# Kernel optimization log

Measured on AMD Instinct MI355X. Metric: run time of the kernel, lower is better.

## Reference

```python
import jax, jax.numpy as jnp
import numpy as np

H = 64   # hidden_size
I = 4    # input_size
O = 1    # output_size

def setup_inputs() -> dict:
    key = jax.random.key(0)
    ks = jax.random.split(key, 7)
    B, T = 1024, 1024
    s = 1.0 / np.sqrt(H)
    x = jax.random.normal(ks[0], (B, T, I), dtype=jnp.float32)
    # PyTorch nn.LSTM params, gate order (i, f, g, o)
    W_ih = jax.random.uniform(ks[1], (4 * H, I), minval=-s, maxval=s, dtype=jnp.float32)
    W_hh = jax.random.uniform(ks[2], (4 * H, H), minval=-s, maxval=s, dtype=jnp.float32)
    b_ih = jax.random.uniform(ks[3], (4 * H,), minval=-s, maxval=s, dtype=jnp.float32)
    b_hh = jax.random.uniform(ks[4], (4 * H,), minval=-s, maxval=s, dtype=jnp.float32)
    W_fc = jax.random.uniform(ks[5], (O, H), minval=-s, maxval=s, dtype=jnp.float32)
    b_fc = jax.random.uniform(ks[6], (O,), minval=-s, maxval=s, dtype=jnp.float32)
    return {"x": x, "W_ih": W_ih, "W_hh": W_hh, "b_ih": b_ih, "b_hh": b_hh,
            "W_fc": W_fc, "b_fc": b_fc}

def _lstm(x, W_ih, W_hh, b_ih, b_hh):
    B, T, _ = x.shape
    # precompute input contribution for all timesteps: [T, B, 4H]
    xg = (jnp.einsum('bti,gi->btg', x, W_ih) + b_ih + b_hh).transpose(1, 0, 2)

    def step(carry, xt):
        h, c = carry
        g = xt + h @ W_hh.T                     # [B, 4H]
        i, f, gg, o = jnp.split(g, 4, axis=-1)  # torch gate order i,f,g,o
        i = jax.nn.sigmoid(i)
        f = jax.nn.sigmoid(f)
        gg = jnp.tanh(gg)
        o = jax.nn.sigmoid(o)
        c = f * c + i * gg
        h = o * jnp.tanh(c)
        return (h, c), h

    h0 = jnp.zeros((B, H), dtype=x.dtype)
    c0 = jnp.zeros((B, H), dtype=x.dtype)
    _, hs = jax.lax.scan(step, (h0, c0), xg)    # hs: [T, B, H]
    return hs.transpose(1, 0, 2)                # [B, T, H]

def reference(x, W_ih, W_hh, b_ih, b_hh, W_fc, b_fc):
    out = _lstm(x, W_ih, W_hh, b_ih, b_hh)      # [B, T, H]
    # dropout in eval mode == identity (deterministic reference)
    return out @ W_fc.T + b_fc                  # [B, T, 1]
```

## Files before the change

### kernel.cpp

```cpp
#include <hip/hip_runtime.h>

#define TLEN  1024
#define HN    64
#define LOG2E 1.4426950408889634f

typedef __fp16 half2v __attribute__((ext_vector_type(2)));


#define FOR16A(X) \
    X(0) X(1) X(2) X(3) X(4) X(5) X(6) X(7) \
    X(8) X(9) X(10) X(11) X(12) X(13) X(14) X(15)
#define FOR16B(X) \
    X(16) X(17) X(18) X(19) X(20) X(21) X(22) X(23) \
    X(24) X(25) X(26) X(27) X(28) X(29) X(30) X(31)
#define FOR32(X) FOR16A(X) FOR16B(X)

__global__ __launch_bounds__(64, 1)
void lstm_dot2(const float* __restrict__ x,
               const float* __restrict__ W_ih,
               const float* __restrict__ W_hh,
               const float* __restrict__ b_ih,
               const float* __restrict__ b_hh,
               const float* __restrict__ W_fc,
               const float* __restrict__ b_fc,
               float* __restrict__ out)
{
    const int b = blockIdx.x;
    const int g = threadIdx.x;

    __shared__ float ring[64][65];

    const float* wr_i = W_hh + (0 * HN + g) * HN;
    const float* wr_f = W_hh + (1 * HN + g) * HN;
    const float* wr_g = W_hh + (2 * HN + g) * HN;
    const float* wr_o = W_hh + (3 * HN + g) * HN;

#define DECL(j) half2v pi##j, pf##j, pg##j, po##j;
    FOR32(DECL)
#undef DECL

#define LOADW(j) \
    pi##j = __builtin_amdgcn_cvt_pkrtz(wr_i[j] * LOG2E, wr_i[(j) + 32] * LOG2E); \
    pf##j = __builtin_amdgcn_cvt_pkrtz(wr_f[j] * LOG2E, wr_f[(j) + 32] * LOG2E); \
    pg##j = __builtin_amdgcn_cvt_pkrtz(wr_g[j] * (2.0f * LOG2E), \
                                       wr_g[(j) + 32] * (2.0f * LOG2E)); \
    po##j = __builtin_amdgcn_cvt_pkrtz(wr_o[j] * LOG2E, wr_o[(j) + 32] * LOG2E); \
    asm volatile("" : "+v"(pi##j), "+v"(pf##j), "+v"(pg##j), "+v"(po##j));
    FOR32(LOADW)
#undef LOADW

    half2v wip0 = __builtin_amdgcn_cvt_pkrtz(W_ih[(0 * HN + g) * 4 + 0] * LOG2E,
                                             W_ih[(0 * HN + g) * 4 + 1] * LOG2E);
    half2v wip1 = __builtin_amdgcn_cvt_pkrtz(W_ih[(0 * HN + g) * 4 + 2] * LOG2E,
                                             W_ih[(0 * HN + g) * 4 + 3] * LOG2E);
    half2v wfp0 = __builtin_amdgcn_cvt_pkrtz(W_ih[(1 * HN + g) * 4 + 0] * LOG2E,
                                             W_ih[(1 * HN + g) * 4 + 1] * LOG2E);
    half2v wfp1 = __builtin_amdgcn_cvt_pkrtz(W_ih[(1 * HN + g) * 4 + 2] * LOG2E,
                                             W_ih[(1 * HN + g) * 4 + 3] * LOG2E);
    half2v wgp0 = __builtin_amdgcn_cvt_pkrtz(W_ih[(2 * HN + g) * 4 + 0] * 2.0f * LOG2E,
                                             W_ih[(2 * HN + g) * 4 + 1] * 2.0f * LOG2E);
    half2v wgp1 = __builtin_amdgcn_cvt_pkrtz(W_ih[(2 * HN + g) * 4 + 2] * 2.0f * LOG2E,
                                             W_ih[(2 * HN + g) * 4 + 3] * 2.0f * LOG2E);
    half2v wop0 = __builtin_amdgcn_cvt_pkrtz(W_ih[(3 * HN + g) * 4 + 0] * LOG2E,
                                             W_ih[(3 * HN + g) * 4 + 1] * LOG2E);
    half2v wop1 = __builtin_amdgcn_cvt_pkrtz(W_ih[(3 * HN + g) * 4 + 2] * LOG2E,
                                             W_ih[(3 * HN + g) * 4 + 3] * LOG2E);

    const float bias_i = (b_ih[0 * HN + g] + b_hh[0 * HN + g]) * LOG2E;
    const float bias_f = (b_ih[1 * HN + g] + b_hh[1 * HN + g]) * LOG2E;
    const float bias_g = (b_ih[2 * HN + g] + b_hh[2 * HN + g]) * (2.0f * LOG2E);
    const float bias_o = (b_ih[3 * HN + g] + b_hh[3 * HN + g]) * LOG2E;
    const float wfc = W_fc[g];
    const float bfc = b_fc[0];

    const float* xb = x   + (size_t)b * TLEN * 4;
    float*       ob = out + (size_t)b * TLEN;

    float h = 0.0f, c = 0.0f;
    int hp = 0;

    float4 xcur = *(const float4*)(xb + (size_t)g * 4);

    for (int ci = 0; ci < TLEN / 64; ++ci) {
        const int cn = (ci < TLEN / 64 - 1) ? ci + 1 : ci;
        float4 xnext = *(const float4*)(xb + (size_t)(cn * 64 + g) * 4);

        const int xq0 = __builtin_bit_cast(int, __builtin_amdgcn_cvt_pkrtz(xcur.x, xcur.y));
        const int xq1 = __builtin_bit_cast(int, __builtin_amdgcn_cvt_pkrtz(xcur.z, xcur.w));

#pragma unroll 2
        for (int s = 0; s < 64; ++s) {
            const int xi0 = __builtin_amdgcn_readlane(xq0, s);
            const int xi1 = __builtin_amdgcn_readlane(xq1, s);
            const half2v xh0 = __builtin_bit_cast(half2v, xi0);
            const half2v xh1 = __builtin_bit_cast(half2v, xi1);

            float ai0 = __builtin_amdgcn_fdot2(wip0, xh0, bias_i, false);
            float af0 = __builtin_amdgcn_fdot2(wfp0, xh0, bias_f, false);
            float ag0 = __builtin_amdgcn_fdot2(wgp0, xh0, bias_g, false);
            float ao0 = __builtin_amdgcn_fdot2(wop0, xh0, bias_o, false);
            float ai1 = __builtin_amdgcn_fdot2(wip1, xh1, 0.0f, false);
            float af1 = __builtin_amdgcn_fdot2(wfp1, xh1, 0.0f, false);
            float ag1 = __builtin_amdgcn_fdot2(wgp1, xh1, 0.0f, false);
            float ao1 = __builtin_amdgcn_fdot2(wop1, xh1, 0.0f, false);

#define MACA(j) { \
            int hj = __builtin_amdgcn_readlane(hp, j); \
            half2v hh = __builtin_bit_cast(half2v, hj); \
            ai0 = __builtin_amdgcn_fdot2(pi##j, hh, ai0, false); \
            af0 = __builtin_amdgcn_fdot2(pf##j, hh, af0, false); \
            ag0 = __builtin_amdgcn_fdot2(pg##j, hh, ag0, false); \
            ao0 = __builtin_amdgcn_fdot2(po##j, hh, ao0, false); }
#define MACB(j) { \
            int hj = __builtin_amdgcn_readlane(hp, j); \
            half2v hh = __builtin_bit_cast(half2v, hj); \
            ai1 = __builtin_amdgcn_fdot2(pi##j, hh, ai1, false); \
            af1 = __builtin_amdgcn_fdot2(pf##j, hh, af1, false); \
            ag1 = __builtin_amdgcn_fdot2(pg##j, hh, ag1, false); \
            ao1 = __builtin_amdgcn_fdot2(po##j, hh, ao1, false); }
            FOR16A(MACA)
            FOR16B(MACB)
#undef MACA
#undef MACB

            const float ai = ai0 + ai1;
            const float af = af0 + af1;
            const float ag = ag0 + ag1;
            const float ao = ao0 + ao1;

            float si = __builtin_amdgcn_rcpf(1.0f + __builtin_amdgcn_exp2f(-ai));
            float sf = __builtin_amdgcn_rcpf(1.0f + __builtin_amdgcn_exp2f(-af));
            float tg = 1.0f - 2.0f * __builtin_amdgcn_rcpf(
                                         1.0f + __builtin_amdgcn_exp2f(ag));
            float so = __builtin_amdgcn_rcpf(1.0f + __builtin_amdgcn_exp2f(-ao));

            c = sf * c + si * tg;
            float th = 1.0f - 2.0f * __builtin_amdgcn_rcpf(
                           1.0f + __builtin_amdgcn_exp2f(c * (2.0f * LOG2E)));
            h = so * th;

            int pd = __builtin_bit_cast(int, h);
            int ps;
            asm("v_mov_b32 %1, %0\n\t"
                "v_permlane32_swap_b32 %0, %1"
                : "+v"(pd), "=&v"(ps));
            const float h_hi = __builtin_bit_cast(float, ps);
            hp = __builtin_bit_cast(int, __builtin_amdgcn_cvt_pkrtz(h, h_hi));

            ring[s][g] = h * wfc;
        }

        __syncthreads();
        float s0 = 0.f, s1 = 0.f, s2 = 0.f, s3 = 0.f;
#pragma unroll
        for (int k = 0; k < HN; k += 4) {
            s0 += ring[g][k];
            s1 += ring[g][k + 1];
            s2 += ring[g][k + 2];
            s3 += ring[g][k + 3];
        }
        ob[ci * 64 + g] = (s0 + s1) + (s2 + s3) + bfc;

        xcur = xnext;
    }
}

extern "C" void kernel_launch(void* const* d_in, const int* in_sizes, int n_in,
                              void* d_out, int out_size, void* d_ws, size_t ws_size,
                              hipStream_t stream) {
    const float* x    = (const float*)d_in[0];
    const float* W_ih = (const float*)d_in[1];
    const float* W_hh = (const float*)d_in[2];
    const float* b_ih = (const float*)d_in[3];
    const float* b_hh = (const float*)d_in[4];
    const float* W_fc = (const float*)d_in[5];
    const float* b_fc = (const float*)d_in[6];
    float* out = (float*)d_out;

    const int B = in_sizes[0] / (TLEN * 4);
    lstm_dot2<<<dim3(B), dim3(64), 0, stream>>>(
        x, W_ih, W_hh, b_ih, b_hh, W_fc, b_fc, out);
}
```

Before: 653.3 us.

## Split LSTM hidden units across two waves with LDS-exchanged hidden state

```diff
diff --git a/kernel.cpp b/kernel.cpp
--- a/kernel.cpp
+++ b/kernel.cpp
@@ -7,126 +7,153 @@
 typedef __fp16 half2v __attribute__((ext_vector_type(2)));
 
 
-#define FOR16A(X) \
+#define FOR16(X) \
     X(0) X(1) X(2) X(3) X(4) X(5) X(6) X(7) \
     X(8) X(9) X(10) X(11) X(12) X(13) X(14) X(15)
-#define FOR16B(X) \
-    X(16) X(17) X(18) X(19) X(20) X(21) X(22) X(23) \
-    X(24) X(25) X(26) X(27) X(28) X(29) X(30) X(31)
-#define FOR32(X) FOR16A(X) FOR16B(X)
-
-__global__ __launch_bounds__(64, 1)
-void lstm_dot2(const float* __restrict__ x,
-               const float* __restrict__ W_ih,
-               const float* __restrict__ W_hh,
-               const float* __restrict__ b_ih,
-               const float* __restrict__ b_hh,
-               const float* __restrict__ W_fc,
-               const float* __restrict__ b_fc,
-               float* __restrict__ out)
+
+__global__ __launch_bounds__(128, 1)
+void lstm_2wave(const float* __restrict__ x,
+                const float* __restrict__ W_ih,
+                const float* __restrict__ W_hh,
+                const float* __restrict__ b_ih,
+                const float* __restrict__ b_hh,
+                const float* __restrict__ W_fc,
+                const float* __restrict__ b_fc,
+                float* __restrict__ out)
 {
-    const int b = blockIdx.x;
-    const int g = threadIdx.x;
-
+    const int b    = blockIdx.x;
+    const int tid  = threadIdx.x;
+    const int l    = tid & 63;
+    const int w    = tid >> 6;
+    const int lh   = l & 31;
+    const int half = l >> 5;
+    const int u    = w * 32 + lh;
+
+    __shared__ alignas(16) unsigned short hbuf[2][HN];
     __shared__ float ring[64][65];
 
-    const float* wr_i = W_hh + (0 * HN + g) * HN;
-    const float* wr_f = W_hh + (1 * HN + g) * HN;
-    const float* wr_g = W_hh + (2 * HN + g) * HN;
-    const float* wr_o = W_hh + (3 * HN + g) * HN;
-
-#define DECL(j) half2v pi##j, pf##j, pg##j, po##j;
-    FOR32(DECL)
+    if (tid < HN) { hbuf[0][tid] = 0; hbuf[1][tid] = 0; }
+
+    const float* wr_i = W_hh + (0 * HN + u) * HN;
+    const float* wr_f = W_hh + (1 * HN + u) * HN;
+    const float* wr_g = W_hh + (2 * HN + u) * HN;
+    const float* wr_o = W_hh + (3 * HN + u) * HN;
+
+#define DECL(p) half2v pi##p, pf##p, pg##p, po##p;
+    FOR16(DECL)
 #undef DECL
 
-#define LOADW(j) \
-    pi##j = __builtin_amdgcn_cvt_pkrtz(wr_i[j] * LOG2E, wr_i[(j) + 32] * LOG2E); \
-    pf##j = __builtin_amdgcn_cvt_pkrtz(wr_f[j] * LOG2E, wr_f[(j) + 32] * LOG2E); \
-    pg##j = __builtin_amdgcn_cvt_pkrtz(wr_g[j] * (2.0f * LOG2E), \
-                                       wr_g[(j) + 32] * (2.0f * LOG2E)); \
-    po##j = __builtin_amdgcn_cvt_pkrtz(wr_o[j] * LOG2E, wr_o[(j) + 32] * LOG2E); \
-    asm volatile("" : "+v"(pi##j), "+v"(pf##j), "+v"(pg##j), "+v"(po##j));
-    FOR32(LOADW)
+#define LOADW(p) { \
+    const int j0 = (half * 16 + (p)) * 2, j1 = j0 + 1; \
+    pi##p = __builtin_amdgcn_cvt_pkrtz(wr_i[j0] * LOG2E, wr_i[j1] * LOG2E); \
+    pf##p = __builtin_amdgcn_cvt_pkrtz(wr_f[j0] * LOG2E, wr_f[j1] * LOG2E); \
+    pg##p = __builtin_amdgcn_cvt_pkrtz(wr_g[j0] * (2.0f * LOG2E), \
+                                       wr_g[j1] * (2.0f * LOG2E)); \
+    po##p = __builtin_amdgcn_cvt_pkrtz(wr_o[j0] * LOG2E, wr_o[j1] * LOG2E); \
+    asm volatile("" : "+v"(pi##p), "+v"(pf##p), "+v"(pg##p), "+v"(po##p)); }
+    FOR16(LOADW)
 #undef LOADW
 
-    half2v wip0 = __builtin_amdgcn_cvt_pkrtz(W_ih[(0 * HN + g) * 4 + 0] * LOG2E,
-                                             W_ih[(0 * HN + g) * 4 + 1] * LOG2E);
-    half2v wip1 = __builtin_amdgcn_cvt_pkrtz(W_ih[(0 * HN + g) * 4 + 2] * LOG2E,
-                                             W_ih[(0 * HN + g) * 4 + 3] * LOG2E);
-    half2v wfp0 = __builtin_amdgcn_cvt_pkrtz(W_ih[(1 * HN + g) * 4 + 0] * LOG2E,
-                                             W_ih[(1 * HN + g) * 4 + 1] * LOG2E);
-    half2v wfp1 = __builtin_amdgcn_cvt_pkrtz(W_ih[(1 * HN + g) * 4 + 2] * LOG2E,
-                                             W_ih[(1 * HN + g) * 4 + 3] * LOG2E);
-    half2v wgp0 = __builtin_amdgcn_cvt_pkrtz(W_ih[(2 * HN + g) * 4 + 0] * 2.0f * LOG2E,
-                                             W_ih[(2 * HN + g) * 4 + 1] * 2.0f * LOG2E);
-    half2v wgp1 = __builtin_amdgcn_cvt_pkrtz(W_ih[(2 * HN + g) * 4 + 2] * 2.0f * LOG2E,
-                                             W_ih[(2 * HN + g) * 4 + 3] * 2.0f * LOG2E);
-    half2v wop0 = __builtin_amdgcn_cvt_pkrtz(W_ih[(3 * HN + g) * 4 + 0] * LOG2E,
-                                             W_ih[(3 * HN + g) * 4 + 1] * LOG2E);
-    half2v wop1 = __builtin_amdgcn_cvt_pkrtz(W_ih[(3 * HN + g) * 4 + 2] * LOG2E,
-                                             W_ih[(3 * HN + g) * 4 + 3] * LOG2E);
-
-    const float bias_i = (b_ih[0 * HN + g] + b_hh[0 * HN + g]) * LOG2E;
-    const float bias_f = (b_ih[1 * HN + g] + b_hh[1 * HN + g]) * LOG2E;
-    const float bias_g = (b_ih[2 * HN + g] + b_hh[2 * HN + g]) * (2.0f * LOG2E);
-    const float bias_o = (b_ih[3 * HN + g] + b_hh[3 * HN + g]) * LOG2E;
-    const float wfc = W_fc[g];
+    const float xs = 0.5f * LOG2E;
+    half2v wip0 = __builtin_amdgcn_cvt_pkrtz(W_ih[(0 * HN + u) * 4 + 0] * xs,
+                                             W_ih[(0 * HN + u) * 4 + 1] * xs);
+    half2v wip1 = __builtin_amdgcn_cvt_pkrtz(W_ih[(0 * HN + u) * 4 + 2] * xs,
+                                             W_ih[(0 * HN + u) * 4 + 3] * xs);
+    half2v wfp0 = __builtin_amdgcn_cvt_pkrtz(W_ih[(1 * HN + u) * 4 + 0] * xs,
+                                             W_ih[(1 * HN + u) * 4 + 1] * xs);
+    half2v wfp1 = __builtin_amdgcn_cvt_pkrtz(W_ih[(1 * HN + u) * 4 + 2] * xs,
+                                             W_ih[(1 * HN + u) * 4 + 3] * xs);
+    half2v wgp0 = __builtin_amdgcn_cvt_pkrtz(W_ih[(2 * HN + u) * 4 + 0] * LOG2E,
+                                             W_ih[(2 * HN + u) * 4 + 1] * LOG2E);
+    half2v wgp1 = __builtin_amdgcn_cvt_pkrtz(W_ih[(2 * HN + u) * 4 + 2] * LOG2E,
+                                             W_ih[(2 * HN + u) * 4 + 3] * LOG2E);
+    half2v wop0 = __builtin_amdgcn_cvt_pkrtz(W_ih[(3 * HN + u) * 4 + 0] * xs,
+                                             W_ih[(3 * HN + u) * 4 + 1] * xs);
+    half2v wop1 = __builtin_amdgcn_cvt_pkrtz(W_ih[(3 * HN + u) * 4 + 2] * xs,
+                                             W_ih[(3 * HN + u) * 4 + 3] * xs);
+
+    const float bias_i = 0.5f * (b_ih[0 * HN + u] + b_hh[0 * HN + u]) * LOG2E;
+    const float bias_f = 0.5f * (b_ih[1 * HN + u] + b_hh[1 * HN + u]) * LOG2E;
+    const float bias_g =        (b_ih[2 * HN + u] + b_hh[2 * HN + u]) * LOG2E;
+    const float bias_o = 0.5f * (b_ih[3 * HN + u] + b_hh[3 * HN + u]) * LOG2E;
+    const float wfc = W_fc[u];
     const float bfc = b_fc[0];
 
     const float* xb = x   + (size_t)b * TLEN * 4;
     float*       ob = out + (size_t)b * TLEN;
 
     float h = 0.0f, c = 0.0f;
-    int hp = 0;
-
-    float4 xcur = *(const float4*)(xb + (size_t)g * 4);
+
+    float4 xcur = *(const float4*)(xb + (size_t)l * 4);
+
+    const unsigned char* hbase = (const unsigned char*)hbuf;
+
+    __syncthreads();
 
     for (int ci = 0; ci < TLEN / 64; ++ci) {
         const int cn = (ci < TLEN / 64 - 1) ? ci + 1 : ci;
-        float4 xnext = *(const float4*)(xb + (size_t)(cn * 64 + g) * 4);
+        float4 xnext = *(const float4*)(xb + (size_t)(cn * 64 + l) * 4);
 
         const int xq0 = __builtin_bit_cast(int, __builtin_amdgcn_cvt_pkrtz(xcur.x, xcur.y));
         const int xq1 = __builtin_bit_cast(int, __builtin_amdgcn_cvt_pkrtz(xcur.z, xcur.w));
 
 #pragma unroll 2
         for (int s = 0; s < 64; ++s) {
+            const uint4* hb = (const uint4*)(hbase + ((s & 1) ^ 1) * 128
+                                                   + half * 64);
+            const uint4 r0 = hb[0];
+            const uint4 r1 = hb[1];
+            const uint4 r2 = hb[2];
+            const uint4 r3 = hb[3];
+
             const int xi0 = __builtin_amdgcn_readlane(xq0, s);
             const int xi1 = __builtin_amdgcn_readlane(xq1, s);
             const half2v xh0 = __builtin_bit_cast(half2v, xi0);
             const half2v xh1 = __builtin_bit_cast(half2v, xi1);
 
-            float ai0 = __builtin_amdgcn_fdot2(wip0, xh0, bias_i, false);
-            float af0 = __builtin_amdgcn_fdot2(wfp0, xh0, bias_f, false);
-            float ag0 = __builtin_amdgcn_fdot2(wgp0, xh0, bias_g, false);
-            float ao0 = __builtin_amdgcn_fdot2(wop0, xh0, bias_o, false);
-            float ai1 = __builtin_amdgcn_fdot2(wip1, xh1, 0.0f, false);
-            float af1 = __builtin_amdgcn_fdot2(wfp1, xh1, 0.0f, false);
-            float ag1 = __builtin_amdgcn_fdot2(wgp1, xh1, 0.0f, false);
-            float ao1 = __builtin_amdgcn_fdot2(wop1, xh1, 0.0f, false);
-
-#define MACA(j) { \
-            int hj = __builtin_amdgcn_readlane(hp, j); \
-            half2v hh = __builtin_bit_cast(half2v, hj); \
-            ai0 = __builtin_amdgcn_fdot2(pi##j, hh, ai0, false); \
-            af0 = __builtin_amdgcn_fdot2(pf##j, hh, af0, false); \
-            ag0 = __builtin_amdgcn_fdot2(pg##j, hh, ag0, false); \
-            ao0 = __builtin_amdgcn_fdot2(po##j, hh, ao0, false); }
-#define MACB(j) { \
-            int hj = __builtin_amdgcn_readlane(hp, j); \
-            half2v hh = __builtin_bit_cast(half2v, hj); \
-            ai1 = __builtin_amdgcn_fdot2(pi##j, hh, ai1, false); \
-            af1 = __builtin_amdgcn_fdot2(pf##j, hh, af1, false); \
-            ag1 = __builtin_amdgcn_fdot2(pg##j, hh, ag1, false); \
-            ao1 = __builtin_amdgcn_fdot2(po##j, hh, ao1, false); }
-            FOR16A(MACA)
-            FOR16B(MACB)
-#undef MACA
-#undef MACB
-
-            const float ai = ai0 + ai1;
-            const float af = af0 + af1;
-            const float ag = ag0 + ag1;
-            const float ao = ao0 + ao1;
+            float aiA = __builtin_amdgcn_fdot2(wip0, xh0, bias_i, false);
+            float afA = __builtin_amdgcn_fdot2(wfp0, xh0, bias_f, false);
+            float agA = __builtin_amdgcn_fdot2(wgp0, xh0, bias_g, false);
+            float aoA = __builtin_amdgcn_fdot2(wop0, xh0, bias_o, false);
+            aiA = __builtin_amdgcn_fdot2(wip1, xh1, aiA, false);
+            afA = __builtin_amdgcn_fdot2(wfp1, xh1, afA, false);
+            agA = __builtin_amdgcn_fdot2(wgp1, xh1, agA, false);
+            aoA = __builtin_amdgcn_fdot2(wop1, xh1, aoA, false);
+            float aiB = 0.0f, afB = 0.0f, agB = 0.0f, aoB = 0.0f;
+
+#define MAC_A(p, cmp) { const half2v hh = __builtin_bit_cast(half2v, cmp); \
+            aiA = __builtin_amdgcn_fdot2(pi##p, hh, aiA, false); \
+            afA = __builtin_amdgcn_fdot2(pf##p, hh, afA, false); \
+            agA = __builtin_amdgcn_fdot2(pg##p, hh, agA, false); \
+            aoA = __builtin_amdgcn_fdot2(po##p, hh, aoA, false); }
+#define MAC_B(p, cmp) { const half2v hh = __builtin_bit_cast(half2v, cmp); \
+            aiB = __builtin_amdgcn_fdot2(pi##p, hh, aiB, false); \
+            afB = __builtin_amdgcn_fdot2(pf##p, hh, afB, false); \
+            agB = __builtin_amdgcn_fdot2(pg##p, hh, agB, false); \
+            aoB = __builtin_amdgcn_fdot2(po##p, hh, aoB, false); }
+            MAC_A(0,  r0.x) MAC_B(8,  r2.x)
+            MAC_A(1,  r0.y) MAC_B(9,  r2.y)
+            MAC_A(2,  r0.z) MAC_B(10, r2.z)
+            MAC_A(3,  r0.w) MAC_B(11, r2.w)
+            MAC_A(4,  r1.x) MAC_B(12, r3.x)
+            MAC_A(5,  r1.y) MAC_B(13, r3.y)
+            MAC_A(6,  r1.z) MAC_B(14, r3.z)
+            MAC_A(7,  r1.w) MAC_B(15, r3.w)
+#undef MAC_A
+#undef MAC_B
+
+            float ai = aiA + aiB;
+            float af = afA + afB;
+            float ag = agA + agB;
+            float ao = aoA + aoB;
+#define COMBINE(a) { \
+            int pd = __builtin_bit_cast(int, a); int ps; \
+            asm("v_mov_b32 %1, %0\n\t" \
+                "v_permlane32_swap_b32 %0, %1" \
+                : "+v"(pd), "=&v"(ps)); \
+            a += __builtin_bit_cast(float, ps); }
+            COMBINE(ai) COMBINE(af) COMBINE(ag) COMBINE(ao)
+#undef COMBINE
 
             float si = __builtin_amdgcn_rcpf(1.0f + __builtin_amdgcn_exp2f(-ai));
             float sf = __builtin_amdgcn_rcpf(1.0f + __builtin_amdgcn_exp2f(-af));
@@ -139,27 +166,27 @@
                            1.0f + __builtin_amdgcn_exp2f(c * (2.0f * LOG2E)));
             h = so * th;
 
-            int pd = __builtin_bit_cast(int, h);
-            int ps;
-            asm("v_mov_b32 %1, %0\n\t"
-                "v_permlane32_swap_b32 %0, %1"
-                : "+v"(pd), "=&v"(ps));
-            const float h_hi = __builtin_bit_cast(float, ps);
-            hp = __builtin_bit_cast(int, __builtin_amdgcn_cvt_pkrtz(h, h_hi));
-
-            ring[s][g] = h * wfc;
+            const int hpk = __builtin_bit_cast(int,
+                                __builtin_amdgcn_cvt_pkrtz(h, h));
+            if (half == 0) {
+                hbuf[s & 1][u] = (unsigned short)(hpk & 0xffff);
+                ring[s][u] = h * wfc;
+            }
+            __syncthreads();
         }
 
+        if (tid < 64) {
+            float s0 = 0.f, s1 = 0.f, s2 = 0.f, s3 = 0.f;
+#pragma unroll
+            for (int k = 0; k < HN; k += 4) {
+                s0 += ring[tid][k];
+                s1 += ring[tid][k + 1];
+                s2 += ring[tid][k + 2];
+                s3 += ring[tid][k + 3];
+            }
+            ob[ci * 64 + tid] = (s0 + s1) + (s2 + s3) + bfc;
+        }
         __syncthreads();
-        float s0 = 0.f, s1 = 0.f, s2 = 0.f, s3 = 0.f;
-#pragma unroll
-        for (int k = 0; k < HN; k += 4) {
-            s0 += ring[g][k];
-            s1 += ring[g][k + 1];
-            s2 += ring[g][k + 2];
-            s3 += ring[g][k + 3];
-        }
-        ob[ci * 64 + g] = (s0 + s1) + (s2 + s3) + bfc;
 
         xcur = xnext;
     }
@@ -178,6 +205,6 @@
     float* out = (float*)d_out;
 
     const int B = in_sizes[0] / (TLEN * 4);
-    lstm_dot2<<<dim3(B), dim3(64), 0, stream>>>(
+    lstm_2wave<<<dim3(B), dim3(128), 0, stream>>>(
         x, W_ih, W_hh, b_ih, b_hh, W_fc, b_fc, out);
 }
```

After: 697.0 us. 6.7% more time.
